# Kernel optimization log

Hardware: AMD Instinct MI355X
Metric: run time of the kernel (lower is better)

## Reference

```python
import jax, jax.numpy as jnp
import numpy as np

DIM = 1024
N_HEADS = 16
HEAD_DIM = DIM // N_HEADS


def setup_inputs() -> dict:
    key = jax.random.key(0)
    kx, kq, kk, kv, ko = jax.random.split(key, 5)
    B, S = 2, 2048
    scale = 1.0 / np.sqrt(DIM)
    return {
        "x": jax.random.normal(kx, (B, S, DIM), dtype=jnp.float32),
        "Wq": jax.random.normal(kq, (DIM, DIM), dtype=jnp.float32) * scale,
        "Wk": jax.random.normal(kk, (DIM, DIM), dtype=jnp.float32) * scale,
        "Wv": jax.random.normal(kv, (DIM, DIM), dtype=jnp.float32) * scale,
        "Wo": jax.random.normal(ko, (DIM, DIM), dtype=jnp.float32) * scale,
    }


def rotate_half(x):
    x1, x2 = jnp.split(x, 2, axis=-1)
    return jnp.concatenate([-x2, x1], axis=-1)


def rope_freqs(seq_len, dim):
    inv_freq = 1.0 / (10000.0 ** (jnp.arange(0, dim, 2, dtype=jnp.float32) / dim))
    t = jnp.arange(seq_len, dtype=jnp.float32)
    freqs = jnp.einsum('i,j->ij', t, inv_freq)  # [S, dim/2]
    return jnp.concatenate([freqs, freqs], axis=-1)  # [S, dim]


def apply_rotary(x, freqs):
    # x: [B, H, S, Dh], freqs: [S, Dh]
    cos = jnp.cos(freqs)[None, None]
    sin = jnp.sin(freqs)[None, None]
    return x * cos + rotate_half(x) * sin


def reference(x, Wq, Wk, Wv, Wo):
    B, S, D = x.shape
    H, Dh = N_HEADS, HEAD_DIM
    # nn.Linear(dim, dim, bias=False): y = x @ W.T
    q = (x @ Wq.T).reshape(B, S, H, Dh).transpose(0, 2, 1, 3)
    k = (x @ Wk.T).reshape(B, S, H, Dh).transpose(0, 2, 1, 3)
    v = (x @ Wv.T).reshape(B, S, H, Dh).transpose(0, 2, 1, 3)
    freqs = rope_freqs(S, Dh)
    q = apply_rotary(q, freqs)
    k = apply_rotary(k, freqs)
    attn = jnp.einsum('bhqd,bhkd->bhqk', q, k) / jnp.sqrt(jnp.float32(Dh))
    attn = jax.nn.softmax(attn, axis=-1)
    out = jnp.einsum('bhqk,bhkd->bhqd', attn, v)
    out = out.transpose(0, 2, 1, 3).reshape(B, S, D)
    return out @ Wo.T
```

## Files before the change

kernel.cpp:

```cpp
#include <hip/hip_runtime.h>
#include <hip/hip_bf16.h>

#define NB 2
#define NS 2048
#define ND 1024
#define NH 16
#define NDH 64
#define NM 4096

typedef __bf16 bf16;
typedef __bf16 bf16x8 __attribute__((ext_vector_type(8)));
typedef __bf16 bf16x4 __attribute__((ext_vector_type(4)));
typedef float f32x4 __attribute__((ext_vector_type(4)));
typedef float f32x16 __attribute__((ext_vector_type(16)));

#define ASYNC16(g, l) __builtin_amdgcn_global_load_lds( \
    (const __attribute__((address_space(1))) void*)(g), \
    (__attribute__((address_space(3))) void*)(l), 16, 0, 0)

static __device__ __forceinline__ unsigned cvt_pk_bf16(float a, float b) {
  unsigned r;
  asm("v_cvt_pk_bf16_f32 %0, %1, %2" : "=v"(r) : "v"(a), "v"(b));
  return r;
}

__global__ __launch_bounds__(256) void convert_kernel(
    const float* __restrict__ x,
    const float* __restrict__ wq, const float* __restrict__ wk,
    const float* __restrict__ wv, const float* __restrict__ wo,
    bf16* __restrict__ xb, bf16* __restrict__ wb) {
  int i = blockIdx.x * 256 + threadIdx.x;
  const int n_x4 = (NM * ND) / 4;
  const int n_w4 = (ND * ND) / 4;
  float4 v;
  bf16* dst;
  if (i < n_x4) {
    v = ((const float4*)x)[i];
    dst = xb + (size_t)i * 4;
  } else {
    int j = i - n_x4;
    int w = j / n_w4;
    int o = j - w * n_w4;
    const float* W = (w == 0) ? wq : (w == 1) ? wk : (w == 2) ? wv : wo;
    v = ((const float4*)W)[o];
    dst = wb + (size_t)w * (ND * ND) + (size_t)o * 4;
  }
  bf16x4 o4;
  o4[0] = (bf16)v.x; o4[1] = (bf16)v.y; o4[2] = (bf16)v.z; o4[3] = (bf16)v.w;
  *(bf16x4*)dst = o4;
}

__global__ __launch_bounds__(256) void tab_kernel(float2* __restrict__ tab) {
  int t = blockIdx.x * 256 + threadIdx.x;
  int s = t >> 5, d = t & 31;
  float invf = exp2f(-0.4152410118609203f * (float)d);
  float f = (float)s * invf;
  float sn, cs;
  sincosf(f, &sn, &cs);
  tab[t] = make_float2(cs, sn);
}

__global__ __launch_bounds__(256) void gemm_qkv(
    const bf16* __restrict__ A, const bf16* __restrict__ Bmat,
    bf16* __restrict__ Qr, bf16* __restrict__ Kr, bf16* __restrict__ vraw,
    const float2* __restrict__ tab) {
  __shared__ bf16 As[128 * 64];
  __shared__ bf16 Bs[128 * 64];
  const int t = threadIdx.x;
  const int lane = t & 63, w = t >> 6;
  const int wr = w >> 1, wc = w & 1;
  const int bm = blockIdx.y * 128;
  const int bn = blockIdx.x * 128;
  const int z = blockIdx.z;
  const bf16* Bz = Bmat + (size_t)z * ND * ND;

  f32x4 acc[4][4];
#pragma unroll
  for (int i = 0; i < 4; ++i)
#pragma unroll
    for (int j = 0; j < 4; ++j) acc[i][j] = (f32x4){0.f, 0.f, 0.f, 0.f};

  for (int kt = 0; kt < ND / 64; ++kt) {
    __syncthreads();
#pragma unroll
    for (int i = 0; i < 4; ++i) {
      int c = w * 64 + lane + i * 256;
      int row = c >> 3;
      int js = (c & 7) ^ (row & 7);
      ASYNC16(A + (size_t)(bm + row) * ND + kt * 64 + js * 8, As + c * 8);
      ASYNC16(Bz + (size_t)(bn + row) * ND + kt * 64 + js * 8, Bs + c * 8);
    }
    __syncthreads();
#pragma unroll
    for (int ks = 0; ks < 2; ++ks) {
      const int kb = ks * 64 + (lane >> 4) * 16;
      bf16x8 af[4], bfr[4];
#pragma unroll
      for (int i = 0; i < 4; ++i) {
        int ra = wr * 64 + i * 16 + (lane & 15);
        af[i] = *(const bf16x8*)((const char*)As + ra * 128 + (kb ^ ((ra & 7) << 4)));
        int rb = wc * 64 + i * 16 + (lane & 15);
        bfr[i] = *(const bf16x8*)((const char*)Bs + rb * 128 + (kb ^ ((rb & 7) << 4)));
      }
#pragma unroll
      for (int i = 0; i < 4; ++i)
#pragma unroll
        for (int j = 0; j < 4; ++j)
          acc[i][j] = __builtin_amdgcn_mfma_f32_16x16x32_bf16(af[i], bfr[j], acc[i][j], 0, 0, 0);
    }
  }

  const int row0 = bm + wr * 64;
  const int col0 = bn + wc * 64;
  if (z == 2) {
#pragma unroll
    for (int i = 0; i < 4; ++i)
#pragma unroll
      for (int j = 0; j < 4; ++j) {
        int r = row0 + i * 16 + (lane >> 4) * 4;
        int ccol = col0 + j * 16 + (lane & 15);
#pragma unroll
        for (int q = 0; q < 4; ++q)
          vraw[(size_t)(r + q) * ND + ccol] = (bf16)acc[i][j][q];
      }
  } else {
    bf16* dst = z ? Kr : Qr;
    const float qs = z ? 1.0f : 0.125f;
    const int h = col0 >> 6;
    const int ln15 = lane & 15;
#pragma unroll
    for (int i = 0; i < 4; ++i)
#pragma unroll
      for (int j = 0; j < 2; ++j)
#pragma unroll
        for (int q = 0; q < 4; ++q) {
          int r = row0 + i * 16 + (lane >> 4) * 4 + q;
          int b = r >> 11, s = r & (NS - 1);
          int d1 = j * 16 + ln15;
          float2 tc = tab[s * 32 + d1];
          float x1 = acc[i][j][q], x2 = acc[i][j + 2][q];
          size_t base = ((size_t)((b * NH + h) * NS + s)) * NDH;
          dst[base + d1]      = (bf16)((x1 * tc.x - x2 * tc.y) * qs);
          dst[base + d1 + 32] = (bf16)((x2 * tc.x + x1 * tc.y) * qs);
        }
  }
}

__global__ __launch_bounds__(256) void gemm_out(
    const bf16* __restrict__ A, const bf16* __restrict__ Bmat,
    float* __restrict__ Cout) {
  __shared__ bf16 As[128 * 64];
  __shared__ bf16 Bs[128 * 64];
  const int t = threadIdx.x;
  const int lane = t & 63, w = t >> 6;
  const int wr = w >> 1, wc = w & 1;
  const int bm = blockIdx.y * 128;
  const int bn = blockIdx.x * 128;

  f32x4 acc[4][4];
#pragma unroll
  for (int i = 0; i < 4; ++i)
#pragma unroll
    for (int j = 0; j < 4; ++j) acc[i][j] = (f32x4){0.f, 0.f, 0.f, 0.f};

  for (int kt = 0; kt < ND / 64; ++kt) {
    __syncthreads();
#pragma unroll
    for (int i = 0; i < 4; ++i) {
      int c = w * 64 + lane + i * 256;
      int row = c >> 3;
      int js = (c & 7) ^ (row & 7);
      ASYNC16(A + (size_t)(bm + row) * ND + kt * 64 + js * 8, As + c * 8);
      ASYNC16(Bmat + (size_t)(bn + row) * ND + kt * 64 + js * 8, Bs + c * 8);
    }
    __syncthreads();
#pragma unroll
    for (int ks = 0; ks < 2; ++ks) {
      const int kb = ks * 64 + (lane >> 4) * 16;
      bf16x8 af[4], bfr[4];
#pragma unroll
      for (int i = 0; i < 4; ++i) {
        int ra = wr * 64 + i * 16 + (lane & 15);
        af[i] = *(const bf16x8*)((const char*)As + ra * 128 + (kb ^ ((ra & 7) << 4)));
        int rb = wc * 64 + i * 16 + (lane & 15);
        bfr[i] = *(const bf16x8*)((const char*)Bs + rb * 128 + (kb ^ ((rb & 7) << 4)));
      }
#pragma unroll
      for (int i = 0; i < 4; ++i)
#pragma unroll
        for (int j = 0; j < 4; ++j)
          acc[i][j] = __builtin_amdgcn_mfma_f32_16x16x32_bf16(af[i], bfr[j], acc[i][j], 0, 0, 0);
    }
  }

  const int row0 = bm + wr * 64;
  const int col0 = bn + wc * 64;
#pragma unroll
  for (int i = 0; i < 4; ++i)
#pragma unroll
    for (int j = 0; j < 4; ++j) {
      int r = row0 + i * 16 + (lane >> 4) * 4;
      int ccol = col0 + j * 16 + (lane & 15);
#pragma unroll
      for (int q = 0; q < 4; ++q)
        Cout[(size_t)(r + q) * ND + ccol] = acc[i][j][q];
    }
}

__global__ __launch_bounds__(256) void transv_kernel(
    const bf16* __restrict__ vraw, bf16* __restrict__ VT) {
  __shared__ bf16 tl[64][65];
  int s0 = blockIdx.x * 64;
  int bh = blockIdx.y;
  int b = bh >> 4, h = bh & 15;
  int t = threadIdx.x;
#pragma unroll
  for (int i = 0; i < 4; ++i) {
    int row = (t >> 4) + i * 16;
    int d4 = (t & 15) * 4;
    *(bf16x4*)&tl[row][d4] =
        *(const bf16x4*)&vraw[((size_t)(b * NS + s0 + row)) * ND + h * NDH + d4];
  }
  __syncthreads();
#pragma unroll
  for (int i = 0; i < 4; ++i) {
    int dr = (t >> 4) + i * 16;
    int s4 = (t & 15) * 4;
    bf16x4 o;
    o[0] = tl[s4 + 0][dr]; o[1] = tl[s4 + 1][dr];
    o[2] = tl[s4 + 2][dr]; o[3] = tl[s4 + 3][dr];
    *(bf16x4*)&VT[((size_t)(bh * NDH + dr)) * NS + s0 + s4] = o;
  }
}

__global__ __launch_bounds__(256) void attn_kernel(
    const bf16* __restrict__ Qr, const bf16* __restrict__ Kr,
    const bf16* __restrict__ VT, bf16* __restrict__ out) {
  __shared__ bf16 Ks[2][64 * 64];
  __shared__ bf16 Vs[2][64 * 64];
  const int t = threadIdx.x, lane = t & 63, w = t >> 6;
  const int hi = lane >> 5, ln = lane & 31;
  int wg = blockIdx.x;
  int sw = (wg & 7) * 64 + (wg >> 3);
  const int qb = sw & 15, bh = sw >> 4;
  const int q0 = qb * 128 + w * 32;

  bf16x8 qv[4];
  {
    const bf16* Qb = Qr + ((size_t)bh * NS + q0 + ln) * NDH + hi * 8;
#pragma unroll
    for (int c = 0; c < 4; ++c) qv[c] = *(const bf16x8*)(Qb + c * 16);
  }

  f32x16 O0, O1;
#pragma unroll
  for (int r = 0; r < 16; ++r) { O0[r] = 0.f; O1[r] = 0.f; }
  float m = -1e30f, l = 0.f;

#pragma unroll
  for (int i = 0; i < 2; ++i) {
    int ch = t + i * 256;
    int row = ch >> 3, js = (ch & 7) ^ (row & 7);
    ASYNC16(Kr + ((size_t)bh * NS + row) * NDH + js * 8, &Ks[0][ch * 8]);
    ASYNC16(VT + ((size_t)bh * NDH + row) * NS + js * 8, &Vs[0][ch * 8]);
  }
  __syncthreads();

  int cur = 0;
  for (int kt = 0; kt < NS / 64; ++kt) {
    if (kt + 1 < NS / 64) {
      int nb = cur ^ 1;
#pragma unroll
      for (int i = 0; i < 2; ++i) {
        int ch = t + i * 256;
        int row = ch >> 3, js = (ch & 7) ^ (row & 7);
        ASYNC16(Kr + ((size_t)bh * NS + (kt + 1) * 64 + row) * NDH + js * 8, &Ks[nb][ch * 8]);
        ASYNC16(VT + ((size_t)bh * NDH + row) * NS + (kt + 1) * 64 + js * 8, &Vs[nb][ch * 8]);
      }
    }
    const char* Kb = (const char*)Ks[cur];
    const char* Vb = (const char*)Vs[cur];

    f32x16 s0, s1;
#pragma unroll
    for (int r = 0; r < 16; ++r) { s0[r] = 0.f; s1[r] = 0.f; }
#pragma unroll
    for (int c = 0; c < 4; ++c) {
      int ko = c * 32 + hi * 16;
      int r0 = ln, r1 = 32 + ln;
      bf16x8 k0 = *(const bf16x8*)(Kb + r0 * 128 + (ko ^ ((r0 & 7) << 4)));
      bf16x8 k1 = *(const bf16x8*)(Kb + r1 * 128 + (ko ^ ((r1 & 7) << 4)));
      s0 = __builtin_amdgcn_mfma_f32_32x32x16_bf16(k0, qv[c], s0, 0, 0, 0);
      s1 = __builtin_amdgcn_mfma_f32_32x32x16_bf16(k1, qv[c], s1, 0, 0, 0);
    }

    float pmax = s0[0];
#pragma unroll
    for (int r = 1; r < 16; ++r) pmax = fmaxf(pmax, s0[r]);
#pragma unroll
    for (int r = 0; r < 16; ++r) pmax = fmaxf(pmax, s1[r]);
    pmax = fmaxf(pmax, __shfl_xor(pmax, 32, 64));

    if (!__all(pmax - m <= 8.0f)) {
      float mnew = fmaxf(m, pmax);
      float scl = __expf(m - mnew);
      m = mnew; l *= scl;
#pragma unroll
      for (int r = 0; r < 16; ++r) { O0[r] *= scl; O1[r] *= scl; }
    }

    float p0[16], p1[16], sum = 0.f;
#pragma unroll
    for (int r = 0; r < 16; ++r) { p0[r] = __expf(s0[r] - m); sum += p0[r]; }
#pragma unroll
    for (int r = 0; r < 16; ++r) { p1[r] = __expf(s1[r] - m); sum += p1[r]; }
    sum += __shfl_xor(sum, 32, 64);
    l += sum;

    unsigned u0[8], u1[8], x0[8], x1[8];
#pragma unroll
    for (int g = 0; g < 4; ++g) {
      u0[g]     = cvt_pk_bf16(p0[4 * g],     p0[4 * g + 1]);
      u1[g]     = cvt_pk_bf16(p0[4 * g + 2], p0[4 * g + 3]);
      u0[4 + g] = cvt_pk_bf16(p1[4 * g],     p1[4 * g + 1]);
      u1[4 + g] = cvt_pk_bf16(p1[4 * g + 2], p1[4 * g + 3]);
    }
#pragma unroll
    for (int g = 0; g < 8; ++g) {
      x0[g] = __shfl_xor(u0[g], 32, 64);
      x1[g] = __shfl_xor(u1[g], 32, 64);
    }

#pragma unroll
    for (int c = 0; c < 4; ++c) {
      int base = (c >> 1) * 4 + (c & 1) * 2;
      union { unsigned u[4]; bf16x8 v; } pa;
      pa.u[0] = hi ? x0[base + 1] : u0[base];
      pa.u[1] = hi ? x1[base + 1] : u1[base];
      pa.u[2] = hi ? u0[base + 1] : x0[base];
      pa.u[3] = hi ? u1[base + 1] : x1[base];
      int ko = c * 32 + hi * 16;
      int rv0 = ln, rv1 = 32 + ln;
      bf16x8 v0 = *(const bf16x8*)(Vb + rv0 * 128 + (ko ^ ((rv0 & 7) << 4)));
      bf16x8 v1 = *(const bf16x8*)(Vb + rv1 * 128 + (ko ^ ((rv1 & 7) << 4)));
      O0 = __builtin_amdgcn_mfma_f32_32x32x16_bf16(pa.v, v0, O0, 0, 0, 0);
      O1 = __builtin_amdgcn_mfma_f32_32x32x16_bf16(pa.v, v1, O1, 0, 0, 0);
    }

    __syncthreads();
    cur ^= 1;
  }

  float rl = 1.0f / l;
  const int b = bh >> 4, h = bh & 15;
#pragma unroll
  for (int r = 0; r < 16; ++r) {
    int q = (r & 3) + 8 * (r >> 2) + 4 * hi;
    float rlq = __shfl(rl, q, 64);
    int s = q0 + q;
    size_t base = ((size_t)(b * NS + s)) * ND + h * NDH + ln;
    out[base]      = (bf16)(O0[r] * rlq);
    out[base + 32] = (bf16)(O1[r] * rlq);
  }
}

extern "C" void kernel_launch(void* const* d_in, const int* in_sizes, int n_in,
                              void* d_out, int out_size, void* d_ws, size_t ws_size,
                              hipStream_t stream) {
  const float* x  = (const float*)d_in[0];
  const float* wq = (const float*)d_in[1];
  const float* wk = (const float*)d_in[2];
  const float* wv = (const float*)d_in[3];
  const float* wo = (const float*)d_in[4];
  char* ws = (char*)d_ws;
  bf16* xb    = (bf16*)(ws);
  bf16* wb    = (bf16*)(ws + (8u << 20));
  bf16* vraw  = (bf16*)(ws + (16u << 20));
  bf16* Qr    = (bf16*)(ws + (24u << 20));
  bf16* Kr    = (bf16*)(ws + (32u << 20));
  bf16* VT    = (bf16*)(ws + (40u << 20));
  bf16* attnb = (bf16*)(ws + (48u << 20));
  float2* tab = (float2*)(ws + (56u << 20));
  float* out  = (float*)d_out;

  convert_kernel<<<8192, 256, 0, stream>>>(x, wq, wk, wv, wo, xb, wb);
  tab_kernel<<<256, 256, 0, stream>>>(tab);
  gemm_qkv<<<dim3(8, 32, 3), 256, 0, stream>>>(xb, wb, Qr, Kr, vraw, tab);
  transv_kernel<<<dim3(32, 32), 256, 0, stream>>>(vraw, VT);
  attn_kernel<<<dim3(512), 256, 0, stream>>>(Qr, Kr, VT, attnb);
  gemm_out<<<dim3(8, 32), 256, 0, stream>>>(attnb, wb + 3 * ND * ND, out);
}
```

Measured before the change: 216.0 us.

## Load K/V tiles straight from global memory into registers in attention kernel

Removes the LDS double-buffered async staging of K and V tiles and their block-wide barriers. Each wave now loads its K and V fragments directly from global memory into registers, relying on L1/L2 reuse across the four waves. The Q scale also folds in log2(e), so softmax uses exp2f instead of __expf, and the max and sum reductions become trees. The risk is redundant global/L2 traffic with no prefetch to hide load latency, which launch_bounds(256,2) occupancy must absorb.

```diff
diff --git a/kernel.cpp b/kernel.cpp
--- a/kernel.cpp
+++ b/kernel.cpp
@@ -125,7 +125,7 @@
       }
   } else {
     bf16* dst = z ? Kr : Qr;
-    const float qs = z ? 1.0f : 0.125f;
+    const float qs = z ? 1.0f : 0.1803368801111204f;
     const int h = col0 >> 6;
     const int ln15 = lane & 15;
 #pragma unroll
@@ -233,11 +233,9 @@
   }
 }
 
-__global__ __launch_bounds__(256) void attn_kernel(
+__global__ __launch_bounds__(256, 2) void attn_kernel(
     const bf16* __restrict__ Qr, const bf16* __restrict__ Kr,
     const bf16* __restrict__ VT, bf16* __restrict__ out) {
-  __shared__ bf16 Ks[2][64 * 64];
-  __shared__ bf16 Vs[2][64 * 64];
   const int t = threadIdx.x, lane = t & 63, w = t >> 6;
   const int hi = lane >> 5, ln = lane & 31;
   int wg = blockIdx.x;
@@ -252,68 +250,55 @@
     for (int c = 0; c < 4; ++c) qv[c] = *(const bf16x8*)(Qb + c * 16);
   }
 
+  const bf16* kp0 = Kr + ((size_t)bh * NS + ln) * NDH + hi * 8;
+  const bf16* kp1 = kp0 + (size_t)32 * NDH;
+  const bf16* vp0 = VT + ((size_t)bh * NDH + ln) * NS + hi * 8;
+  const bf16* vp1 = vp0 + (size_t)32 * NS;
+
   f32x16 O0, O1;
 #pragma unroll
   for (int r = 0; r < 16; ++r) { O0[r] = 0.f; O1[r] = 0.f; }
   float m = -1e30f, l = 0.f;
 
-#pragma unroll
-  for (int i = 0; i < 2; ++i) {
-    int ch = t + i * 256;
-    int row = ch >> 3, js = (ch & 7) ^ (row & 7);
-    ASYNC16(Kr + ((size_t)bh * NS + row) * NDH + js * 8, &Ks[0][ch * 8]);
-    ASYNC16(VT + ((size_t)bh * NDH + row) * NS + js * 8, &Vs[0][ch * 8]);
-  }
-  __syncthreads();
-
-  int cur = 0;
   for (int kt = 0; kt < NS / 64; ++kt) {
-    if (kt + 1 < NS / 64) {
-      int nb = cur ^ 1;
-#pragma unroll
-      for (int i = 0; i < 2; ++i) {
-        int ch = t + i * 256;
-        int row = ch >> 3, js = (ch & 7) ^ (row & 7);
-        ASYNC16(Kr + ((size_t)bh * NS + (kt + 1) * 64 + row) * NDH + js * 8, &Ks[nb][ch * 8]);
-        ASYNC16(VT + ((size_t)bh * NDH + row) * NS + (kt + 1) * 64 + js * 8, &Vs[nb][ch * 8]);
-      }
-    }
-    const char* Kb = (const char*)Ks[cur];
-    const char* Vb = (const char*)Vs[cur];
-
     f32x16 s0, s1;
 #pragma unroll
     for (int r = 0; r < 16; ++r) { s0[r] = 0.f; s1[r] = 0.f; }
+    bf16x8 k0[4], k1[4];
 #pragma unroll
     for (int c = 0; c < 4; ++c) {
-      int ko = c * 32 + hi * 16;
-      int r0 = ln, r1 = 32 + ln;
-      bf16x8 k0 = *(const bf16x8*)(Kb + r0 * 128 + (ko ^ ((r0 & 7) << 4)));
-      bf16x8 k1 = *(const bf16x8*)(Kb + r1 * 128 + (ko ^ ((r1 & 7) << 4)));
-      s0 = __builtin_amdgcn_mfma_f32_32x32x16_bf16(k0, qv[c], s0, 0, 0, 0);
-      s1 = __builtin_amdgcn_mfma_f32_32x32x16_bf16(k1, qv[c], s1, 0, 0, 0);
-    }
-
-    float pmax = s0[0];
-#pragma unroll
-    for (int r = 1; r < 16; ++r) pmax = fmaxf(pmax, s0[r]);
-#pragma unroll
-    for (int r = 0; r < 16; ++r) pmax = fmaxf(pmax, s1[r]);
+      k0[c] = *(const bf16x8*)(kp0 + c * 16);
+      k1[c] = *(const bf16x8*)(kp1 + c * 16);
+    }
+#pragma unroll
+    for (int c = 0; c < 4; ++c) {
+      s0 = __builtin_amdgcn_mfma_f32_32x32x16_bf16(k0[c], qv[c], s0, 0, 0, 0);
+      s1 = __builtin_amdgcn_mfma_f32_32x32x16_bf16(k1[c], qv[c], s1, 0, 0, 0);
+    }
+
+    float a0[8];
+#pragma unroll
+    for (int r = 0; r < 8; ++r) a0[r] = fmaxf(fmaxf(s0[r], s0[r + 8]), fmaxf(s1[r], s1[r + 8]));
+    float b0 = fmaxf(fmaxf(a0[0], a0[1]), fmaxf(a0[2], a0[3]));
+    float b1 = fmaxf(fmaxf(a0[4], a0[5]), fmaxf(a0[6], a0[7]));
+    float pmax = fmaxf(b0, b1);
     pmax = fmaxf(pmax, __shfl_xor(pmax, 32, 64));
 
     if (!__all(pmax - m <= 8.0f)) {
       float mnew = fmaxf(m, pmax);
-      float scl = __expf(m - mnew);
+      float scl = exp2f(m - mnew);
       m = mnew; l *= scl;
 #pragma unroll
       for (int r = 0; r < 16; ++r) { O0[r] *= scl; O1[r] *= scl; }
     }
 
-    float p0[16], p1[16], sum = 0.f;
-#pragma unroll
-    for (int r = 0; r < 16; ++r) { p0[r] = __expf(s0[r] - m); sum += p0[r]; }
-#pragma unroll
-    for (int r = 0; r < 16; ++r) { p1[r] = __expf(s1[r] - m); sum += p1[r]; }
+    float p0[16], p1[16];
+#pragma unroll
+    for (int r = 0; r < 16; ++r) { p0[r] = exp2f(s0[r] - m); p1[r] = exp2f(s1[r] - m); }
+    float sp[8];
+#pragma unroll
+    for (int r = 0; r < 8; ++r) sp[r] = (p0[r] + p0[r + 8]) + (p1[r] + p1[r + 8]);
+    float sum = (((sp[0] + sp[1]) + (sp[2] + sp[3])) + ((sp[4] + sp[5]) + (sp[6] + sp[7])));
     sum += __shfl_xor(sum, 32, 64);
     l += sum;
 
@@ -331,6 +316,12 @@
       x1[g] = __shfl_xor(u1[g], 32, 64);
     }
 
+    bf16x8 v0[4], v1[4];
+#pragma unroll
+    for (int c = 0; c < 4; ++c) {
+      v0[c] = *(const bf16x8*)(vp0 + c * 16);
+      v1[c] = *(const bf16x8*)(vp1 + c * 16);
+    }
 #pragma unroll
     for (int c = 0; c < 4; ++c) {
       int base = (c >> 1) * 4 + (c & 1) * 2;
@@ -339,16 +330,12 @@
       pa.u[1] = hi ? x1[base + 1] : u1[base];
       pa.u[2] = hi ? u0[base + 1] : x0[base];
       pa.u[3] = hi ? u1[base + 1] : x1[base];
-      int ko = c * 32 + hi * 16;
-      int rv0 = ln, rv1 = 32 + ln;
-      bf16x8 v0 = *(const bf16x8*)(Vb + rv0 * 128 + (ko ^ ((rv0 & 7) << 4)));
-      bf16x8 v1 = *(const bf16x8*)(Vb + rv1 * 128 + (ko ^ ((rv1 & 7) << 4)));
-      O0 = __builtin_amdgcn_mfma_f32_32x32x16_bf16(pa.v, v0, O0, 0, 0, 0);
-      O1 = __builtin_amdgcn_mfma_f32_32x32x16_bf16(pa.v, v1, O1, 0, 0, 0);
-    }
-
-    __syncthreads();
-    cur ^= 1;
+      O0 = __builtin_amdgcn_mfma_f32_32x32x16_bf16(pa.v, v0[c], O0, 0, 0, 0);
+      O1 = __builtin_amdgcn_mfma_f32_32x32x16_bf16(pa.v, v1[c], O1, 0, 0, 0);
+    }
+
+    kp0 += (size_t)64 * NDH; kp1 += (size_t)64 * NDH;
+    vp0 += 64;               vp1 += 64;
   }
 
   float rl = 1.0f / l;
```

New measurement: 276.8 us. 28.2% more time.
